# Kernel tuning notes

Measured on AMD Instinct MI355X. Metric: run time of the kernel, lower is better.

## Reference

```python
import jax, jax.numpy as jnp
import numpy as np

N = 80000       # nodes
E = 1280000     # edges (avg degree 16)
G = 2000        # graphs
NSHAPE, NCOLOR, POSMAX = 16, 16, 1024
HID, OUT, IN_DIM = 64, 2, 40
EPS = 1e-5


def setup_inputs() -> dict:
    key = jax.random.key(0)
    ks = jax.random.split(key, 20)
    f32 = jnp.float32
    return {
        "shape_id": jax.random.randint(ks[0], (N,), 0, NSHAPE),
        "color_id": jax.random.randint(ks[1], (N,), 0, NCOLOR),
        "pos_id": jax.random.randint(ks[2], (N,), 0, POSMAX),
        "edge_index": jax.random.randint(ks[3], (2, E), 0, N),
        "batch": jnp.sort(jax.random.randint(ks[4], (N,), 0, G)),
        "num_graphs": G,
        "shape_tab": jax.random.normal(ks[5], (NSHAPE, 16), f32),
        "color_tab": jax.random.normal(ks[6], (NCOLOR, 16), f32),
        "pos_tab": jax.random.normal(ks[7], (POSMAX, 8), f32),
        "W1l": jax.random.normal(ks[8], (IN_DIM, HID), f32) / np.sqrt(IN_DIM),
        "b1": jnp.zeros((HID,), f32),
        "W1r": jax.random.normal(ks[9], (IN_DIM, HID), f32) / np.sqrt(IN_DIM),
        "g1": jnp.ones((HID,), f32),
        "be1": jnp.zeros((HID,), f32),
        "W2l": jax.random.normal(ks[10], (HID, HID), f32) / np.sqrt(HID),
        "b2": jnp.zeros((HID,), f32),
        "W2r": jax.random.normal(ks[11], (HID, HID), f32) / np.sqrt(HID),
        "g2": jnp.ones((HID,), f32),
        "be2": jnp.zeros((HID,), f32),
        "Wout": jax.random.normal(ks[12], (HID, OUT), f32) / np.sqrt(HID),
        "bout": jnp.zeros((OUT,), f32),
    }


def sage_conv(x, src, dst, Wl, b, Wr, n_nodes):
    # PyG SAGEConv (mean aggr): out = lin_l(mean_{j in N(i)} x_j) + lin_r(x_i)
    agg = jax.ops.segment_sum(x[src], dst, num_segments=n_nodes)     # [N, F]
    deg = jax.ops.segment_sum(jnp.ones((src.shape[0], 1), x.dtype), dst,
                              num_segments=n_nodes)                  # [N, 1]
    agg = agg / jnp.maximum(deg, 1.0)
    return agg @ Wl + b + x @ Wr


def batch_norm(x, gamma, beta):
    # training-mode BatchNorm1d over nodes
    m = x.mean(axis=0)
    v = x.var(axis=0)
    return (x - m) * (gamma / jnp.sqrt(v + EPS)) + beta


def reference(shape_id, color_id, pos_id, edge_index, batch, num_graphs,
              shape_tab, color_tab, pos_tab,
              W1l, b1, W1r, g1, be1,
              W2l, b2, W2r, g2, be2,
              Wout, bout):
    n_nodes = shape_id.shape[0]
    src, dst = edge_index[0], edge_index[1]
    x = jnp.concatenate([shape_tab[shape_id], color_tab[color_id],
                         pos_tab[pos_id]], axis=-1)                  # [N, 40]
    x = jax.nn.relu(batch_norm(sage_conv(x, src, dst, W1l, b1, W1r, n_nodes), g1, be1))
    # dropout: eval mode -> identity
    x = jax.nn.relu(batch_norm(sage_conv(x, src, dst, W2l, b2, W2r, n_nodes), g2, be2))
    # global mean pool over batch segments
    summed = jax.ops.segment_sum(x, batch, num_segments=num_graphs)   # [G, H]
    counts = jax.ops.segment_sum(jnp.ones((n_nodes, 1), x.dtype), batch,
                                 num_segments=num_graphs)
    pooled = summed / jnp.maximum(counts, 1.0)
    return pooled @ Wout + bout                                       # [G, 2]
```

## Files before the change

kernel.cpp:

```cpp
#include <hip/hip_runtime.h>

#define NN 80000
#define NE 1280000
#define NG 2000
#define HID 64
#define FIN1 40
#define BSZ 128
#define NBUK (NN / BSZ)
#define EB 8192
#define NBB ((NE + EB - 1) / EB)
#define NBBP 160
constexpr float EPS = 1e-5f;

typedef _Float16 f16;
typedef f16 f16x8 __attribute__((ext_vector_type(8)));
typedef float f32x4 __attribute__((ext_vector_type(4)));

__global__ void setup(const int* __restrict__ sid, const int* __restrict__ cid,
                      const int* __restrict__ pid, const int* __restrict__ batch,
                      const float* __restrict__ stab, const float* __restrict__ ctab,
                      const float* __restrict__ ptab,
                      const float* __restrict__ W1l, const float* __restrict__ W1r,
                      const float* __restrict__ W2l, const float* __restrict__ W2r,
                      int* __restrict__ ids, f16* __restrict__ Bt1, f16* __restrict__ Bt2,
                      int* __restrict__ gstart,
                      f16* __restrict__ stab16, f16* __restrict__ ctab16,
                      f16* __restrict__ ptab16,
                      float* __restrict__ stats, int* __restrict__ bcnt) {
    int bid = blockIdx.x;
    int tid = threadIdx.x;
    if (bid < 313) {
        int n = bid * 256 + tid;
        if (n < NN) ids[n] = sid[n] | (cid[n] << 4) | (pid[n] << 8);
    } else if (bid < 373) {
        int i = (bid - 313) * 256 + tid;
        if (i < 64 * 104) {
            int j = i / 104, k = i - j * 104;
            float v = 0.f;
            if (k < 40) v = W1l[k * 64 + j];
            else if (k < 80) v = W1r[(k - 40) * 64 + j];
            Bt1[i] = (f16)v;
        }
        int i2 = i - 64 * 104;
        if (i2 >= 0 && i2 < 64 * 136) {
            int j = i2 / 136, k = i2 - j * 136;
            float v = 0.f;
            if (k < 64) v = W2l[k * 64 + j];
            else if (k < 128) v = W2r[(k - 64) * 64 + j];
            Bt2[i2] = (f16)v;
        }
    } else if (bid < 686) {
        int n = (bid - 373) * 256 + tid;
        if (n >= NN) return;
        int cur = batch[n];
        int prev = (n == 0) ? -1 : batch[n - 1];
        for (int g = prev + 1; g <= cur; g++) gstart[g] = n;
        if (n == NN - 1)
            for (int g = cur + 1; g <= NG; g++) gstart[g] = NN;
    } else if (bid < 720) {
        int i = (bid - 686) * 256 + tid;
        if (i < 256) stab16[i] = (f16)stab[i];
        else if (i < 512) ctab16[i - 256] = (f16)ctab[i - 256];
        else if (i < 512 + 8192) ptab16[i - 512] = (f16)ptab[i - 512];
    } else {
        if (tid < 256) stats[tid] = 0.f;
        for (int i = tid; i < NBUK; i += 256) bcnt[i] = 0;
    }
}

__global__ void khist(const int* __restrict__ dst, int* __restrict__ bhistT,
                      int* __restrict__ bcnt) {
    __shared__ int lh[NBUK];
    for (int i = threadIdx.x; i < NBUK; i += 256) lh[i] = 0;
    __syncthreads();
    int e0 = blockIdx.x * EB, e1 = min(e0 + EB, NE);
    for (int e = e0 + threadIdx.x; e < e1; e += 256) atomicAdd(&lh[dst[e] >> 7], 1);
    __syncthreads();
    for (int i = threadIdx.x; i < NBUK; i += 256) {
        int c = lh[i];
        bhistT[i * NBBP + blockIdx.x] = c;
        if (c) atomicAdd(&bcnt[i], c);
    }
}

__global__ void kscan_a(const int* __restrict__ bcnt, int* __restrict__ bstart) {
    __shared__ int l[1024];
    int t = threadIdx.x;
    l[t] = (t < NBUK) ? bcnt[t] : 0;
    __syncthreads();
    for (int off = 1; off < 1024; off <<= 1) {
        int v = (t >= off) ? l[t - off] : 0;
        __syncthreads();
        l[t] += v;
        __syncthreads();
    }
    if (t < NBUK) bstart[t] = (t == 0) ? 0 : l[t - 1];
    if (t == NBUK) bstart[NBUK] = NE;
}

__global__ void kscan_b(const int* __restrict__ bhistT, const int* __restrict__ bstart,
                        int* __restrict__ lbaseT) {
    int b = blockIdx.x;
    int l = threadIdx.x;
    int run = bstart[b];
    for (int i0 = 0; i0 < NBB; i0 += 64) {
        int idx = i0 + l;
        int v = (idx < NBB) ? bhistT[b * NBBP + idx] : 0;
        int inc = v;
        for (int off = 1; off < 64; off <<= 1) {
            int tt = __shfl_up(inc, off);
            if (l >= off) inc += tt;
        }
        if (idx < NBB) lbaseT[b * NBBP + idx] = run + inc - v;
        run += __shfl(inc, 63);
    }
}

__global__ void kbin(const int* __restrict__ src, const int* __restrict__ dst,
                     const int* __restrict__ lbaseT, int* __restrict__ ebuf) {
    __shared__ int lcur[NBUK];
    for (int i = threadIdx.x; i < NBUK; i += 256) lcur[i] = lbaseT[i * NBBP + blockIdx.x];
    __syncthreads();
    int e0 = blockIdx.x * EB, e1 = min(e0 + EB, NE);
    for (int e = e0 + threadIdx.x; e < e1; e += 256) {
        int d = dst[e];
        int off = atomicAdd(&lcur[d >> 7], 1);
        ebuf[off] = (src[e] << 7) | (d & 127);
    }
}

__global__ void kfill(const int* __restrict__ ebuf, const int* __restrict__ bstart,
                      int* __restrict__ row_ptr, int* __restrict__ eidx) {
    __shared__ int cnt[BSZ];
    __shared__ int sb[BSZ];
    __shared__ int lcur[BSZ];
    int b = blockIdx.x, t = threadIdx.x;
    int nbase = b << 7;
    if (t < BSZ) cnt[t] = 0;
    __syncthreads();
    int s0 = bstart[b], s1 = bstart[b + 1];
    for (int i = s0 + t; i < s1; i += 256) atomicAdd(&cnt[ebuf[i] & 127], 1);
    __syncthreads();
    if (t < BSZ) sb[t] = cnt[t];
    __syncthreads();
    for (int off = 1; off < BSZ; off <<= 1) {
        int v = (t >= off && t < BSZ) ? sb[t - off] : 0;
        __syncthreads();
        if (t < BSZ) sb[t] += v;
        __syncthreads();
    }
    if (t < BSZ) {
        int excl = ((t == 0) ? 0 : sb[t - 1]) + s0;
        row_ptr[nbase + t] = excl;
        lcur[t] = excl;
    }
    if (b == 0 && t == 0) row_ptr[NN] = NE;
    __syncthreads();
    for (int i = s0 + t; i < s1; i += 256) {
        int v = ebuf[i];
        int pos = atomicAdd(&lcur[v & 127], 1);
        eidx[pos] = v >> 7;
    }
}

__global__ void gather1(const int* __restrict__ row_ptr, const int* __restrict__ eidx,
                        const int* __restrict__ ids,
                        const f16* __restrict__ stab16, const f16* __restrict__ ctab16,
                        const f16* __restrict__ ptab16, f16* __restrict__ agg) {
    int tt = blockIdx.x * 256 + threadIdx.x;
    int n = tt >> 6;
    int lane = threadIdx.x & 63;
    if (n >= NN) return;
    int grp = lane >> 3, li = lane & 7;
    bool act = li < 5;
    int beg = row_ptr[n], end = row_ptr[n + 1];
    f16x8 ach;
#pragma unroll
    for (int i = 0; i < 8; i++) ach[i] = (f16)0.f;
    for (int j0 = beg; j0 < end; j0 += 64) {
        int cnt = min(64, end - j0);
        int myid = (j0 + lane < end) ? eidx[j0 + lane] : 0;
        int steps = (cnt + 7) >> 3;
        for (int u = 0; u < steps; u++) {
            int e = u * 8 + grp;
            int s = __shfl(myid, e);
            if (e < cnt && act) {
                int id = ids[s];
                const f16* rowp;
                if (li < 2)      rowp = &stab16[(id & 15) * 16 + li * 8];
                else if (li < 4) rowp = &ctab16[((id >> 4) & 15) * 16 + (li - 2) * 8];
                else             rowp = &ptab16[(id >> 8) * 8];
                ach += *(const f16x8*)rowp;
            }
        }
    }
    float ac[8];
#pragma unroll
    for (int i = 0; i < 8; i++) ac[i] = (float)ach[i];
#pragma unroll
    for (int m = 8; m <= 32; m <<= 1) {
#pragma unroll
        for (int i = 0; i < 8; i++) ac[i] += __shfl_xor(ac[i], m);
    }
    if (lane < 5) {
        float inv = 1.0f / (float)max(end - beg, 1);
        f16x8 o;
#pragma unroll
        for (int i = 0; i < 8; i++) o[i] = (f16)(ac[i] * inv);
        *(f16x8*)&agg[(size_t)n * FIN1 + lane * 8] = o;
    }
}

__global__ void bn_apply16(f16* __restrict__ h, const float* __restrict__ stats,
                           const float* __restrict__ g, const float* __restrict__ be) {
    __shared__ float ssc[64], ssh[64];
    int tid = threadIdx.x;
    if (tid < 64) {
        const float invn = 1.0f / (float)NN;
        float m = stats[tid] * invn;
        float var = stats[64 + tid] * invn - m * m;
        float sc = g[tid] * __frsqrt_rn(var + EPS);
        ssc[tid] = sc;
        ssh[tid] = be[tid] - m * sc;
    }
    __syncthreads();
    int idx = blockIdx.x * 256 + tid;
    if (idx >= NN * 8) return;
    int f = (idx & 7) * 8;
    f16x8 v = *(f16x8*)&h[(size_t)idx * 8];
    f16x8 o;
#pragma unroll
    for (int i = 0; i < 8; i++) {
        float xv = (float)v[i];
        o[i] = (f16)fmaxf(fmaf(xv, ssc[f + i], ssh[f + i]), 0.f);
    }
    *(f16x8*)&h[(size_t)idx * 8] = o;
}

__global__ void gather2(const int* __restrict__ row_ptr, const int* __restrict__ eidx,
                        const f16* __restrict__ x, f16* __restrict__ agg) {
    int tt = blockIdx.x * 256 + threadIdx.x;
    int n = tt >> 6;
    int lane = threadIdx.x & 63;
    if (n >= NN) return;
    int grp = lane >> 3;
    int fl = (lane & 7) * 8;
    int beg = row_ptr[n], end = row_ptr[n + 1];
    f16x8 ach;
#pragma unroll
    for (int i = 0; i < 8; i++) ach[i] = (f16)0.f;
    for (int j0 = beg; j0 < end; j0 += 64) {
        int cnt = min(64, end - j0);
        int myid = (j0 + lane < end) ? eidx[j0 + lane] : 0;
        int steps = (cnt + 7) >> 3;
        for (int u = 0; u < steps; u++) {
            int e = u * 8 + grp;
            int s = __shfl(myid, e);
            if (e < cnt) {
                ach += *(const f16x8*)&x[(size_t)s * HID + fl];
            }
        }
    }
    float ac[8];
#pragma unroll
    for (int i = 0; i < 8; i++) ac[i] = (float)ach[i];
#pragma unroll
    for (int m = 8; m <= 32; m <<= 1) {
#pragma unroll
        for (int i = 0; i < 8; i++) ac[i] += __shfl_xor(ac[i], m);
    }
    if (lane < 8) {
        float inv = 1.0f / (float)max(end - beg, 1);
        f16x8 o;
#pragma unroll
        for (int i = 0; i < 8; i++) o[i] = (f16)(ac[i] * inv);
        *(f16x8*)&agg[(size_t)n * HID + fl] = o;
    }
}

__launch_bounds__(256)
__global__ void sage_mfma1(const int* __restrict__ ids, const f16* __restrict__ aggv,
                           const f16* __restrict__ stab16, const f16* __restrict__ ctab16,
                           const f16* __restrict__ ptab16,
                           const f16* __restrict__ Btg, const float* __restrict__ bias,
                           f16* __restrict__ h, float* __restrict__ stats) {
    __shared__ float sred[4][64];
    __shared__ float qred[4][64];
    const int KP = 104;

    int tid = threadIdx.x;
    int n0 = blockIdx.x * 64;
    int w = tid >> 6, l = tid & 63;
    int jloc = l & 15, kg = l >> 4;
    int n = n0 + w * 16 + jloc;

    f16x8 af[3];
#pragma unroll
    for (int kk = 0; kk < 3; kk++) {
        int c = kk * 4 + kg;
        if (c < 5) {
            af[kk] = *(const f16x8*)&aggv[(size_t)n * FIN1 + c * 8];
        } else if (c < 10) {
            int id = ids[n];
            int cc = c - 5;
            const f16* rowp;
            if (cc < 2)      rowp = &stab16[(id & 15) * 16 + cc * 8];
            else if (cc < 4) rowp = &ctab16[((id >> 4) & 15) * 16 + (cc - 2) * 8];
            else             rowp = &ptab16[(id >> 8) * 8];
            af[kk] = *(const f16x8*)rowp;
        } else {
#pragma unroll
            for (int i = 0; i < 8; i++) af[kk][i] = (f16)0.f;
        }
    }

    f32x4 acc[4];
#pragma unroll
    for (int jt = 0; jt < 4; jt++) {
        float bj = bias[jt * 16 + jloc];
        acc[jt] = (f32x4){bj, bj, bj, bj};
    }
#pragma unroll
    for (int kk = 0; kk < 3; kk++) {
#pragma unroll
        for (int jt = 0; jt < 4; jt++) {
            f16x8 bf = *(const f16x8*)&Btg[(jt * 16 + jloc) * KP + kk * 32 + kg * 8];
            acc[jt] = __builtin_amdgcn_mfma_f32_16x16x32_f16(af[kk], bf, acc[jt], 0, 0, 0);
        }
    }
#pragma unroll
    for (int jt = 0; jt < 4; jt++) {
        float sv = 0.f, qv = 0.f;
#pragma unroll
        for (int reg = 0; reg < 4; reg++) {
            f16 hv = (f16)acc[jt][reg];
            int nn2 = n0 + w * 16 + kg * 4 + reg;
            h[(size_t)nn2 * HID + jt * 16 + jloc] = hv;
            float v = (float)hv;
            sv += v; qv += v * v;
        }
        sv += __shfl_xor(sv, 16); sv += __shfl_xor(sv, 32);
        qv += __shfl_xor(qv, 16); qv += __shfl_xor(qv, 32);
        if (kg == 0) { sred[w][jt * 16 + jloc] = sv; qred[w][jt * 16 + jloc] = qv; }
    }
    __syncthreads();
    if (tid < 128) {
        int f2 = tid & 63, which = tid >> 6;
        float r = which ? (qred[0][f2] + qred[1][f2] + qred[2][f2] + qred[3][f2])
                        : (sred[0][f2] + sred[1][f2] + sred[2][f2] + sred[3][f2]);
        atomicAdd(&stats[which * 64 + f2], r);
    }
}

__launch_bounds__(256)
__global__ void sage_mfma2(const f16* __restrict__ x, const f16* __restrict__ aggv,
                           const f16* __restrict__ Btg, const float* __restrict__ bias,
                           f16* __restrict__ h, float* __restrict__ stats) {
    __shared__ float sred[4][64];
    __shared__ float qred[4][64];
    const int KP = 136;

    int tid = threadIdx.x;
    int n0 = blockIdx.x * 64;
    int w = tid >> 6, l = tid & 63;
    int jloc = l & 15, kg = l >> 4;
    int n = n0 + w * 16 + jloc;

    f16x8 af[4];
#pragma unroll
    for (int kk = 0; kk < 4; kk++) {
        int c = kk * 4 + kg;
        if (c < 8) af[kk] = *(const f16x8*)&aggv[(size_t)n * HID + c * 8];
        else       af[kk] = *(const f16x8*)&x[(size_t)n * HID + (c - 8) * 8];
    }

    f32x4 acc[4];
#pragma unroll
    for (int jt = 0; jt < 4; jt++) {
        float bj = bias[jt * 16 + jloc];
        acc[jt] = (f32x4){bj, bj, bj, bj};
    }
#pragma unroll
    for (int kk = 0; kk < 4; kk++) {
#pragma unroll
        for (int jt = 0; jt < 4; jt++) {
            f16x8 bf = *(const f16x8*)&Btg[(jt * 16 + jloc) * KP + kk * 32 + kg * 8];
            acc[jt] = __builtin_amdgcn_mfma_f32_16x16x32_f16(af[kk], bf, acc[jt], 0, 0, 0);
        }
    }
#pragma unroll
    for (int jt = 0; jt < 4; jt++) {
        float sv = 0.f, qv = 0.f;
#pragma unroll
        for (int reg = 0; reg < 4; reg++) {
            f16 hv = (f16)acc[jt][reg];
            int nn2 = n0 + w * 16 + kg * 4 + reg;
            h[(size_t)nn2 * HID + jt * 16 + jloc] = hv;
            float v = (float)hv;
            sv += v; qv += v * v;
        }
        sv += __shfl_xor(sv, 16); sv += __shfl_xor(sv, 32);
        qv += __shfl_xor(qv, 16); qv += __shfl_xor(qv, 32);
        if (kg == 0) { sred[w][jt * 16 + jloc] = sv; qred[w][jt * 16 + jloc] = qv; }
    }
    __syncthreads();
    if (tid < 128) {
        int f2 = tid & 63, which = tid >> 6;
        float r = which ? (qred[0][f2] + qred[1][f2] + qred[2][f2] + qred[3][f2])
                        : (sred[0][f2] + sred[1][f2] + sred[2][f2] + sred[3][f2]);
        atomicAdd(&stats[which * 64 + f2], r);
    }
}

__global__ void pool_out(const f16* __restrict__ h, const float* __restrict__ stats2,
                         const float* __restrict__ g2, const float* __restrict__ be2,
                         const int* __restrict__ gstart,
                         const float* __restrict__ Wout, const float* __restrict__ bout,
                         float* __restrict__ out) {
    int w = (blockIdx.x * blockDim.x + threadIdx.x) >> 6;
    int f = threadIdx.x & 63;
    if (w >= NG) return;
    const float invn = 1.0f / (float)NN;
    float m = stats2[f] * invn;
    float var = stats2[64 + f] * invn - m * m;
    float sc = g2[f] / sqrtf(var + EPS);
    float sh = be2[f] - m * sc;
    int n0 = gstart[w], n1 = gstart[w + 1];
    float acc = 0.f;
    for (int n = n0; n < n1; n++) {
        float v = fmaf((float)h[(size_t)n * HID + f], sc, sh);
        acc += fmaxf(v, 0.0f);
    }
    float inv = 1.0f / (float)max(n1 - n0, 1);
    float p = acc * inv;
    float a0 = p * Wout[f * 2 + 0];
    float a1 = p * Wout[f * 2 + 1];
#pragma unroll
    for (int mm = 1; mm < 64; mm <<= 1) {
        a0 += __shfl_xor(a0, mm);
        a1 += __shfl_xor(a1, mm);
    }
    if (f == 0) {
        out[w * 2 + 0] = a0 + bout[0];
        out[w * 2 + 1] = a1 + bout[1];
    }
}

extern "C" void kernel_launch(void* const* d_in, const int* in_sizes, int n_in,
                              void* d_out, int out_size, void* d_ws, size_t ws_size,
                              hipStream_t stream) {
    const int* sid = (const int*)d_in[0];
    const int* cid = (const int*)d_in[1];
    const int* pid = (const int*)d_in[2];
    const int* ei = (const int*)d_in[3];
    const int* batch = (const int*)d_in[4];
    const float* stab = (const float*)d_in[6];
    const float* ctab = (const float*)d_in[7];
    const float* ptab = (const float*)d_in[8];
    const float* W1l = (const float*)d_in[9];
    const float* b1 = (const float*)d_in[10];
    const float* W1r = (const float*)d_in[11];
    const float* g1 = (const float*)d_in[12];
    const float* be1 = (const float*)d_in[13];
    const float* W2l = (const float*)d_in[14];
    const float* b2 = (const float*)d_in[15];
    const float* W2r = (const float*)d_in[16];
    const float* g2 = (const float*)d_in[17];
    const float* be2 = (const float*)d_in[18];
    const float* Wout = (const float*)d_in[19];
    const float* bout = (const float*)d_in[20];

    const int* src = ei;
    const int* dst = ei + NE;

    char* p = (char*)d_ws;
    f16* agg = (f16*)p;        p += (size_t)NN * HID * 2;
    f16* h1 = (f16*)p;         p += (size_t)NN * HID * 2;
    f16* h2 = (f16*)p;         p += (size_t)NN * HID * 2;
    f16* bt1 = (f16*)p;        p += 64 * 104 * 2;
    f16* bt2 = (f16*)p;        p += 64 * 136 * 2;
    f16* stab16 = (f16*)p;     p += 256 * 2;
    f16* ctab16 = (f16*)p;     p += 256 * 2;
    f16* ptab16 = (f16*)p;     p += 8192 * 2;
    float* stats = (float*)p;  p += 256 * 4;
    int* bcnt = (int*)p;       p += NBUK * 4;
    int* ids = (int*)p;        p += (size_t)NN * 4;
    int* row_ptr = (int*)p;    p += (NN + 1) * 4;
    int* gstart = (int*)p;     p += (NG + 1) * 4;
    int* bstart = (int*)p;     p += (NBUK + 1) * 4;
    int* bhistT = (int*)p;     p += (size_t)NBUK * NBBP * 4;
    int* lbaseT = (int*)p;     p += (size_t)NBUK * NBBP * 4;
    int* ebuf = (int*)p;       p += (size_t)NE * 4;
    int* eidx = (int*)p;       p += (size_t)NE * 4;

    const int B = 256;

    setup<<<721, B, 0, stream>>>(sid, cid, pid, batch, stab, ctab, ptab,
                                 W1l, W1r, W2l, W2r,
                                 ids, bt1, bt2, gstart, stab16, ctab16, ptab16,
                                 stats, bcnt);

    khist<<<NBB, B, 0, stream>>>(dst, bhistT, bcnt);
    kscan_a<<<1, 1024, 0, stream>>>(bcnt, bstart);
    kscan_b<<<NBUK, 64, 0, stream>>>(bhistT, bstart, lbaseT);
    kbin<<<NBB, B, 0, stream>>>(src, dst, lbaseT, ebuf);
    kfill<<<NBUK, B, 0, stream>>>(ebuf, bstart, row_ptr, eidx);

    gather1<<<(NN * 64 + B - 1) / B, B, 0, stream>>>(row_ptr, eidx, ids,
                                                     stab16, ctab16, ptab16, agg);
    sage_mfma1<<<NN / 64, B, 0, stream>>>(ids, agg, stab16, ctab16, ptab16,
                                          bt1, b1, h1, stats);
    bn_apply16<<<(NN * 8 + B - 1) / B, B, 0, stream>>>(h1, stats, g1, be1);

    gather2<<<(NN * 64 + B - 1) / B, B, 0, stream>>>(row_ptr, eidx, h1, agg);
    sage_mfma2<<<NN / 64, B, 0, stream>>>(h1, agg, bt2, b2, h2, stats + 128);

    pool_out<<<(NG * 64 + B - 1) / B, B, 0, stream>>>(h2, stats + 128, g2, be2, gstart,
                                                      Wout, bout, (float*)d_out);
}
```

Before: 228.1 us.

## Fold histogram into setup, merge scans, and parallelize pooling per graph

The edge-bucket histogram is merged into the setup kernel as extra blocks. The two scan kernels are combined into one, where each bucket block computes its own prefix by summing the earlier bucket counts. The bcnt array is now zeroed with a memset ahead of the launch. Pooling moves from one wavefront per graph to a 256-thread block per graph that splits nodes across four wavefronts and reduces in shared memory. This removes two kernel launches and serialization, at the cost of redundant prefix work (each block reads up to 625 counts) and more blocks in pooling.

```diff
diff --git a/kernel.cpp b/kernel.cpp
--- a/kernel.cpp
+++ b/kernel.cpp
@@ -16,17 +16,20 @@
 typedef f16 f16x8 __attribute__((ext_vector_type(8)));
 typedef float f32x4 __attribute__((ext_vector_type(4)));
 
-__global__ void setup(const int* __restrict__ sid, const int* __restrict__ cid,
-                      const int* __restrict__ pid, const int* __restrict__ batch,
-                      const float* __restrict__ stab, const float* __restrict__ ctab,
-                      const float* __restrict__ ptab,
-                      const float* __restrict__ W1l, const float* __restrict__ W1r,
-                      const float* __restrict__ W2l, const float* __restrict__ W2r,
-                      int* __restrict__ ids, f16* __restrict__ Bt1, f16* __restrict__ Bt2,
-                      int* __restrict__ gstart,
-                      f16* __restrict__ stab16, f16* __restrict__ ctab16,
-                      f16* __restrict__ ptab16,
-                      float* __restrict__ stats, int* __restrict__ bcnt) {
+__global__ void setup2(const int* __restrict__ sid, const int* __restrict__ cid,
+                       const int* __restrict__ pid, const int* __restrict__ batch,
+                       const float* __restrict__ stab, const float* __restrict__ ctab,
+                       const float* __restrict__ ptab,
+                       const float* __restrict__ W1l, const float* __restrict__ W1r,
+                       const float* __restrict__ W2l, const float* __restrict__ W2r,
+                       const int* __restrict__ dst,
+                       int* __restrict__ ids, f16* __restrict__ Bt1, f16* __restrict__ Bt2,
+                       int* __restrict__ gstart,
+                       f16* __restrict__ stab16, f16* __restrict__ ctab16,
+                       f16* __restrict__ ptab16,
+                       float* __restrict__ stats,
+                       int* __restrict__ bhistT, int* __restrict__ bcnt) {
+    __shared__ int lh[NBUK];
     int bid = blockIdx.x;
     int tid = threadIdx.x;
     if (bid < 313) {
@@ -62,51 +65,39 @@
         if (i < 256) stab16[i] = (f16)stab[i];
         else if (i < 512) ctab16[i - 256] = (f16)ctab[i - 256];
         else if (i < 512 + 8192) ptab16[i - 512] = (f16)ptab[i - 512];
+    } else if (bid == 720) {
+        if (tid < 256) stats[tid] = 0.f;
     } else {
-        if (tid < 256) stats[tid] = 0.f;
-        for (int i = tid; i < NBUK; i += 256) bcnt[i] = 0;
-    }
-}
-
-__global__ void khist(const int* __restrict__ dst, int* __restrict__ bhistT,
-                      int* __restrict__ bcnt) {
-    __shared__ int lh[NBUK];
-    for (int i = threadIdx.x; i < NBUK; i += 256) lh[i] = 0;
-    __syncthreads();
-    int e0 = blockIdx.x * EB, e1 = min(e0 + EB, NE);
-    for (int e = e0 + threadIdx.x; e < e1; e += 256) atomicAdd(&lh[dst[e] >> 7], 1);
-    __syncthreads();
-    for (int i = threadIdx.x; i < NBUK; i += 256) {
-        int c = lh[i];
-        bhistT[i * NBBP + blockIdx.x] = c;
-        if (c) atomicAdd(&bcnt[i], c);
-    }
-}
-
-__global__ void kscan_a(const int* __restrict__ bcnt, int* __restrict__ bstart) {
-    __shared__ int l[1024];
-    int t = threadIdx.x;
-    l[t] = (t < NBUK) ? bcnt[t] : 0;
-    __syncthreads();
-    for (int off = 1; off < 1024; off <<= 1) {
-        int v = (t >= off) ? l[t - off] : 0;
+        int kb = bid - 721;
+        for (int i = tid; i < NBUK; i += 256) lh[i] = 0;
         __syncthreads();
-        l[t] += v;
+        int e0 = kb * EB, e1 = min(e0 + EB, NE);
+        for (int e = e0 + tid; e < e1; e += 256) atomicAdd(&lh[dst[e] >> 7], 1);
         __syncthreads();
-    }
-    if (t < NBUK) bstart[t] = (t == 0) ? 0 : l[t - 1];
-    if (t == NBUK) bstart[NBUK] = NE;
-}
-
-__global__ void kscan_b(const int* __restrict__ bhistT, const int* __restrict__ bstart,
-                        int* __restrict__ lbaseT) {
+        for (int i = tid; i < NBUK; i += 256) {
+            int c = lh[i];
+            bhistT[i * NBBP + kb] = c;
+            if (c) atomicAdd(&bcnt[i], c);
+        }
+    }
+}
+
+__global__ void kscan(const int* __restrict__ bcnt, const int* __restrict__ bhistT,
+                      int* __restrict__ bstart, int* __restrict__ lbaseT) {
     int b = blockIdx.x;
     int l = threadIdx.x;
-    int run = bstart[b];
+    int s = 0;
+    for (int i = l; i < b; i += 64) s += bcnt[i];
+#pragma unroll
+    for (int off = 1; off < 64; off <<= 1) s += __shfl_xor(s, off);
+    if (l == 0) bstart[b] = s;
+    if (b == 0 && l == 0) bstart[NBUK] = NE;
+    int run = s;
     for (int i0 = 0; i0 < NBB; i0 += 64) {
         int idx = i0 + l;
         int v = (idx < NBB) ? bhistT[b * NBBP + idx] : 0;
         int inc = v;
+#pragma unroll
         for (int off = 1; off < 64; off <<= 1) {
             int tt = __shfl_up(inc, off);
             if (l >= off) inc += tt;
@@ -417,9 +408,10 @@
                          const int* __restrict__ gstart,
                          const float* __restrict__ Wout, const float* __restrict__ bout,
                          float* __restrict__ out) {
-    int w = (blockIdx.x * blockDim.x + threadIdx.x) >> 6;
-    int f = threadIdx.x & 63;
-    if (w >= NG) return;
+    __shared__ float red[4][64];
+    int w = blockIdx.x;
+    int tid = threadIdx.x;
+    int f = tid & 63, seg = tid >> 6;
     const float invn = 1.0f / (float)NN;
     float m = stats2[f] * invn;
     float var = stats2[64 + f] * invn - m * m;
@@ -427,22 +419,27 @@
     float sh = be2[f] - m * sc;
     int n0 = gstart[w], n1 = gstart[w + 1];
     float acc = 0.f;
-    for (int n = n0; n < n1; n++) {
+    for (int n = n0 + seg; n < n1; n += 4) {
         float v = fmaf((float)h[(size_t)n * HID + f], sc, sh);
         acc += fmaxf(v, 0.0f);
     }
-    float inv = 1.0f / (float)max(n1 - n0, 1);
-    float p = acc * inv;
-    float a0 = p * Wout[f * 2 + 0];
-    float a1 = p * Wout[f * 2 + 1];
-#pragma unroll
-    for (int mm = 1; mm < 64; mm <<= 1) {
-        a0 += __shfl_xor(a0, mm);
-        a1 += __shfl_xor(a1, mm);
-    }
-    if (f == 0) {
-        out[w * 2 + 0] = a0 + bout[0];
-        out[w * 2 + 1] = a1 + bout[1];
+    red[seg][f] = acc;
+    __syncthreads();
+    if (seg == 0) {
+        acc = red[0][f] + red[1][f] + red[2][f] + red[3][f];
+        float inv = 1.0f / (float)max(n1 - n0, 1);
+        float p = acc * inv;
+        float a0 = p * Wout[f * 2 + 0];
+        float a1 = p * Wout[f * 2 + 1];
+#pragma unroll
+        for (int mm = 1; mm < 64; mm <<= 1) {
+            a0 += __shfl_xor(a0, mm);
+            a1 += __shfl_xor(a1, mm);
+        }
+        if (f == 0) {
+            out[w * 2 + 0] = a0 + bout[0];
+            out[w * 2 + 1] = a1 + bout[1];
+        }
     }
 }
 
@@ -495,14 +492,14 @@
 
     const int B = 256;
 
-    setup<<<721, B, 0, stream>>>(sid, cid, pid, batch, stab, ctab, ptab,
-                                 W1l, W1r, W2l, W2r,
-                                 ids, bt1, bt2, gstart, stab16, ctab16, ptab16,
-                                 stats, bcnt);
-
-    khist<<<NBB, B, 0, stream>>>(dst, bhistT, bcnt);
-    kscan_a<<<1, 1024, 0, stream>>>(bcnt, bstart);
-    kscan_b<<<NBUK, 64, 0, stream>>>(bhistT, bstart, lbaseT);
+    hipMemsetAsync(bcnt, 0, NBUK * sizeof(int), stream);
+
+    setup2<<<721 + NBB, B, 0, stream>>>(sid, cid, pid, batch, stab, ctab, ptab,
+                                        W1l, W1r, W2l, W2r, dst,
+                                        ids, bt1, bt2, gstart, stab16, ctab16, ptab16,
+                                        stats, bhistT, bcnt);
+
+    kscan<<<NBUK, 64, 0, stream>>>(bcnt, bhistT, bstart, lbaseT);
     kbin<<<NBB, B, 0, stream>>>(src, dst, lbaseT, ebuf);
     kfill<<<NBUK, B, 0, stream>>>(ebuf, bstart, row_ptr, eidx);
 
@@ -515,6 +512,6 @@
     gather2<<<(NN * 64 + B - 1) / B, B, 0, stream>>>(row_ptr, eidx, h1, agg);
     sage_mfma2<<<NN / 64, B, 0, stream>>>(h1, agg, bt2, b2, h2, stats + 128);
 
-    pool_out<<<(NG * 64 + B - 1) / B, B, 0, stream>>>(h2, stats + 128, g2, be2, gstart,
-                                                      Wout, bout, (float*)d_out);
-}
+    pool_out<<<NG, B, 0, stream>>>(h2, stats + 128, g2, be2, gstart,
+                                   Wout, bout, (float*)d_out);
+}
```

After: 215.5 us. -5.5%, faster.
